# Kernel optimization log

Measured on AMD Instinct MI355X. Metric: run time of the kernel, lower is better.

The kernel has to match this reference:

```python
import jax, jax.numpy as jnp
import numpy as np

T, B, I, H, O = 512, 64, 256, 512, 256

def setup_inputs() -> dict:
    key = jax.random.key(0)
    ks = jax.random.split(key, 7)
    s_ih = 1.0 / np.sqrt(H)
    return {
        "x": jax.random.normal(ks[0], (T, B, I), dtype=jnp.float32),
        "W_ih": jax.random.uniform(ks[1], (H, I), jnp.float32, -s_ih, s_ih),
        "W_hh": jax.random.uniform(ks[2], (H, H), jnp.float32, -s_ih, s_ih),
        "b_ih": jax.random.uniform(ks[3], (H,), jnp.float32, -s_ih, s_ih),
        "b_hh": jax.random.uniform(ks[4], (H,), jnp.float32, -s_ih, s_ih),
        "W_out": jax.random.uniform(ks[5], (O, H), jnp.float32, -s_ih, s_ih),
        "b_out": jax.random.uniform(ks[6], (O,), jnp.float32, -s_ih, s_ih),
    }

def reference(x, W_ih, W_hh, b_ih, b_hh, W_out, b_out):
    # Precompute input projection for all timesteps: [T, B, H]
    xp = jnp.einsum('tbi,hi->tbh', x, W_ih) + b_ih + b_hh

    def step(h, xp_t):
        h_new = jnp.tanh(xp_t + h @ W_hh.T)
        return h_new, h_new

    h0 = jnp.zeros((x.shape[1], W_hh.shape[0]), dtype=x.dtype)
    h_last, rnn_out = jax.lax.scan(step, h0, xp)  # rnn_out: [T, B, H]
    y = jnp.einsum('tbh,oh->tbo', rnn_out, W_out) + b_out
    return y, h_last[None]  # h: [1, B, H] matching torch nn.RNN
```

## Files before the change

kernel.cpp:

```cpp
#include <hip/hip_runtime.h>

#define T_DIM 512
#define B_DIM 64
#define I_DIM 256
#define H_DIM 512
#define O_DIM 256

typedef __attribute__((ext_vector_type(8))) short short8;
typedef __attribute__((ext_vector_type(4))) float f32x4;

__device__ __forceinline__ unsigned short f2bf(float f){
  unsigned int u = __builtin_bit_cast(unsigned int, f);
  u += 0x7fffu + ((u >> 16) & 1u);
  return (unsigned short)(u >> 16);
}
__device__ __forceinline__ float bf2f(unsigned short b){
  unsigned int u = ((unsigned int)b) << 16;
  return __builtin_bit_cast(float, u);
}

#if defined(__has_builtin)
#if __has_builtin(__builtin_amdgcn_sdot4)
#define HAVE_SDOT4 1
#endif
#if __has_builtin(__builtin_amdgcn_update_dpp)
#define HAVE_DPP 1
#endif
#endif

__device__ __forceinline__ int sdot4(int a, int b, int c){
#ifdef HAVE_SDOT4
  return __builtin_amdgcn_sdot4(a, b, c, false);
#else
  #pragma unroll
  for (int i = 0; i < 4; ++i){
    c += (int)(signed char)(a >> (8*i) & 0xff) * (int)(signed char)(b >> (8*i) & 0xff);
  }
  return c;
#endif
}

__device__ __forceinline__ int grp8_sum(int v){
#ifdef HAVE_DPP
  v += __builtin_amdgcn_update_dpp(0, v, 0xB1, 0xf, 0xf, true);
  v += __builtin_amdgcn_update_dpp(0, v, 0x4E, 0xf, 0xf, true);
  v += __builtin_amdgcn_update_dpp(0, v, 0x141, 0xf, 0xf, true);
  return v;
#else
  v += __shfl_xor(v, 1);
  v += __shfl_xor(v, 2);
  v += __shfl_xor(v, 4);
  return v;
#endif
}

__global__ void quant_whh(const float* __restrict__ W, int* __restrict__ Wq){
  int p = blockIdx.x * blockDim.x + threadIdx.x;
  const float s  = 0.04419417382415922f;
  const float qs = 127.0f / s;
  int out = 0;
  #pragma unroll
  for (int i = 0; i < 4; ++i){
    float w = W[(size_t)p*4 + i];
    int q = __float2int_rn(w * qs);
    q = q < -127 ? -127 : (q > 127 ? 127 : q);
    out |= (q & 0xff) << (8*i);
  }
  Wq[p] = out;
}

__global__
__attribute__((amdgpu_flat_work_group_size(1024, 1024)))
void rnn_recur(
    const int* __restrict__ Wq,
    const unsigned short* __restrict__ xp,
    unsigned short* __restrict__ rnn,
    float* __restrict__ hlast)
{
  __shared__ int hq[2][128];
  const int b   = blockIdx.x;
  const int tid = threadIdx.x;
  const int g   = tid >> 3;
  const int c   = tid & 7;
  const int row = 4*g + (c & 3);

  int w[4][16];
  #pragma unroll
  for (int i = 0; i < 4; ++i){
    const uint4* wp = (const uint4*)(Wq + (size_t)(4*g + i)*128 + c*16);
    #pragma unroll
    for (int k = 0; k < 4; ++k){
      uint4 v = wp[k];
      w[i][4*k+0] = (int)v.x; w[i][4*k+1] = (int)v.y;
      w[i][4*k+2] = (int)v.z; w[i][4*k+3] = (int)v.w;
    }
  }
  if (tid < 128) hq[0][tid] = 0;

  const int wj = 4*(g >> 4) + 32*((g >> 2) & 3) + (g & 3);

  const float kscale = 0.04419417382415922f / (127.0f * 127.0f);
  const int BH = B_DIM * H_DIM;

  float xp_next = bf2f(xp[(size_t)b*H_DIM + row]);
  __syncthreads();

  for (int t = 0; t < T_DIM; ++t){
    float xp_cur = xp_next;
    {
      int tn = (t + 1 < T_DIM) ? (t + 1) : t;
      xp_next = bf2f(xp[(size_t)tn*BH + (size_t)b*H_DIM + row]);
    }
    const uint4* hb = (const uint4*)hq[t & 1];
    uint4 hv0 = hb[c];
    uint4 hv1 = hb[c + 8];
    uint4 hv2 = hb[c + 16];
    uint4 hv3 = hb[c + 24];

    int acc[4];
    #pragma unroll
    for (int i = 0; i < 4; ++i) acc[i] = 0;
    #pragma unroll
    for (int i = 0; i < 4; ++i){
      acc[i] = sdot4(w[i][ 0], (int)hv0.x, acc[i]);
      acc[i] = sdot4(w[i][ 1], (int)hv0.y, acc[i]);
      acc[i] = sdot4(w[i][ 2], (int)hv0.z, acc[i]);
      acc[i] = sdot4(w[i][ 3], (int)hv0.w, acc[i]);
      acc[i] = sdot4(w[i][ 4], (int)hv1.x, acc[i]);
      acc[i] = sdot4(w[i][ 5], (int)hv1.y, acc[i]);
      acc[i] = sdot4(w[i][ 6], (int)hv1.z, acc[i]);
      acc[i] = sdot4(w[i][ 7], (int)hv1.w, acc[i]);
      acc[i] = sdot4(w[i][ 8], (int)hv2.x, acc[i]);
      acc[i] = sdot4(w[i][ 9], (int)hv2.y, acc[i]);
      acc[i] = sdot4(w[i][10], (int)hv2.z, acc[i]);
      acc[i] = sdot4(w[i][11], (int)hv2.w, acc[i]);
      acc[i] = sdot4(w[i][12], (int)hv3.x, acc[i]);
      acc[i] = sdot4(w[i][13], (int)hv3.y, acc[i]);
      acc[i] = sdot4(w[i][14], (int)hv3.z, acc[i]);
      acc[i] = sdot4(w[i][15], (int)hv3.w, acc[i]);
    }
    #pragma unroll
    for (int i = 0; i < 4; ++i) acc[i] = grp8_sum(acc[i]);

    int t0 = (c & 1) ? acc[1] : acc[0];
    int t1 = (c & 1) ? acc[3] : acc[2];
    int am = (c & 2) ? t1 : t0;

    float pre = xp_cur + (float)am * kscale;
    float aa = fabsf(pre);
    float e  = __expf(-2.0f * aa);
    float r  = (1.0f - e) * __builtin_amdgcn_rcpf(1.0f + e);
    float h  = copysignf(r, pre);

    if ((tid & 7) < 4){
      rnn[(size_t)t*BH + (size_t)b*H_DIM + row] = f2bf(h);
      if (t == T_DIM - 1) hlast[(size_t)b*H_DIM + row] = h;
    }

    int q = __float2int_rn(h * 127.0f) & 0xff;
#ifdef HAVE_DPP
    int p1 = __builtin_amdgcn_update_dpp(0, q, 0xB1, 0xf, 0xf, true);
    int y  = q | (p1 << 8);
    int p2 = __builtin_amdgcn_update_dpp(0, y, 0x4E, 0xf, 0xf, true);
    int z  = y | (p2 << 16);
    if ((tid & 7) == 0) hq[(t + 1) & 1][wj] = z;
#else
    if ((tid & 7) < 4) ((char*)hq[(t + 1) & 1])[wj*4 + c] = (char)q;
#endif
    __syncthreads();
  }
}

template<typename TA, typename TB, typename TO>
__global__ __launch_bounds__(256) void gemm_bt(
    const TA* __restrict__ A, const TB* __restrict__ B, TO* __restrict__ C,
    const float* __restrict__ bias1, const float* __restrict__ bias2,
    int M, int N, int K)
{
  __shared__ unsigned short As[64][40];
  __shared__ unsigned short Bs[64][40];
  const int tid  = threadIdx.x;
  const int m0   = blockIdx.x * 64;
  const int n0   = blockIdx.y * 64;
  const int srow = tid >> 2, skc = tid & 3;
  const int lane = tid & 63, wid = tid >> 6;
  const int wm   = wid >> 1, wn = wid & 1;
  const int lr   = lane & 15, lq = lane >> 4;

  f32x4 acc[2][2];
  #pragma unroll
  for (int i = 0; i < 2; ++i)
    #pragma unroll
    for (int j = 0; j < 2; ++j) acc[i][j] = (f32x4){0.f, 0.f, 0.f, 0.f};

  for (int k0 = 0; k0 < K; k0 += 32){
    {
      const TA* src = A + (size_t)(m0 + srow)*K + k0 + skc*8;
      uint4 v;
      if constexpr (__is_same(TA, float)){
        float4 f0 = *(const float4*)src;
        float4 f1 = *(const float4*)(src + 4);
        v.x = (unsigned)f2bf(f0.x) | ((unsigned)f2bf(f0.y) << 16);
        v.y = (unsigned)f2bf(f0.z) | ((unsigned)f2bf(f0.w) << 16);
        v.z = (unsigned)f2bf(f1.x) | ((unsigned)f2bf(f1.y) << 16);
        v.w = (unsigned)f2bf(f1.z) | ((unsigned)f2bf(f1.w) << 16);
      } else {
        v = *(const uint4*)src;
      }
      *(uint4*)&As[srow][skc*8] = v;
    }
    {
      const TB* src = B + (size_t)(n0 + srow)*K + k0 + skc*8;
      uint4 v;
      if constexpr (__is_same(TB, float)){
        float4 f0 = *(const float4*)src;
        float4 f1 = *(const float4*)(src + 4);
        v.x = (unsigned)f2bf(f0.x) | ((unsigned)f2bf(f0.y) << 16);
        v.y = (unsigned)f2bf(f0.z) | ((unsigned)f2bf(f0.w) << 16);
        v.z = (unsigned)f2bf(f1.x) | ((unsigned)f2bf(f1.y) << 16);
        v.w = (unsigned)f2bf(f1.z) | ((unsigned)f2bf(f1.w) << 16);
      } else {
        v = *(const uint4*)src;
      }
      *(uint4*)&Bs[srow][skc*8] = v;
    }
    __syncthreads();
    uint4 av0 = *(const uint4*)&As[wm*32      + lr][lq*8];
    uint4 av1 = *(const uint4*)&As[wm*32 + 16 + lr][lq*8];
    uint4 bv0 = *(const uint4*)&Bs[wn*32      + lr][lq*8];
    uint4 bv1 = *(const uint4*)&Bs[wn*32 + 16 + lr][lq*8];
    short8 a0 = __builtin_bit_cast(short8, av0);
    short8 a1 = __builtin_bit_cast(short8, av1);
    short8 b0 = __builtin_bit_cast(short8, bv0);
    short8 b1 = __builtin_bit_cast(short8, bv1);
    acc[0][0] = __builtin_amdgcn_mfma_f32_16x16x32_bf16(a0, b0, acc[0][0], 0, 0, 0);
    acc[0][1] = __builtin_amdgcn_mfma_f32_16x16x32_bf16(a0, b1, acc[0][1], 0, 0, 0);
    acc[1][0] = __builtin_amdgcn_mfma_f32_16x16x32_bf16(a1, b0, acc[1][0], 0, 0, 0);
    acc[1][1] = __builtin_amdgcn_mfma_f32_16x16x32_bf16(a1, b1, acc[1][1], 0, 0, 0);
    __syncthreads();
  }

  #pragma unroll
  for (int i = 0; i < 2; ++i)
    #pragma unroll
    for (int j = 0; j < 2; ++j)
      #pragma unroll
      for (int r = 0; r < 4; ++r){
        int grow = m0 + wm*32 + i*16 + lq*4 + r;
        int gcol = n0 + wn*32 + j*16 + lr;
        float v = acc[i][j][r] + bias1[gcol];
        if (bias2) v += bias2[gcol];
        if constexpr (__is_same(TO, float)) C[(size_t)grow*N + gcol] = v;
        else                                C[(size_t)grow*N + gcol] = f2bf(v);
      }
}

extern "C" void kernel_launch(void* const* d_in, const int* in_sizes, int n_in,
                              void* d_out, int out_size, void* d_ws, size_t ws_size,
                              hipStream_t stream){
  (void)in_sizes; (void)n_in; (void)out_size; (void)ws_size;
  const float* x    = (const float*)d_in[0];
  const float* Wih  = (const float*)d_in[1];
  const float* Whh  = (const float*)d_in[2];
  const float* bih  = (const float*)d_in[3];
  const float* bhh  = (const float*)d_in[4];
  const float* Wout = (const float*)d_in[5];
  const float* bout = (const float*)d_in[6];
  float* y     = (float*)d_out;
  float* hlast = y + (size_t)T_DIM * B_DIM * O_DIM;

  char* ws = (char*)d_ws;
  unsigned short* xp  = (unsigned short*)ws;
  unsigned short* rnn = (unsigned short*)(ws + (size_t)32*1024*1024);
  int*            Wq  = (int*)           (ws + (size_t)64*1024*1024);

  quant_whh<<<256, 256, 0, stream>>>(Whh, Wq);
  gemm_bt<float, float, unsigned short><<<dim3(512, 8), 256, 0, stream>>>(
      x, Wih, xp, bih, bhh, T_DIM*B_DIM, H_DIM, I_DIM);
  rnn_recur<<<64, 1024, 0, stream>>>(Wq, xp, rnn, hlast);
  gemm_bt<unsigned short, float, float><<<dim3(512, 4), 256, 0, stream>>>(
      rnn, Wout, y, bout, nullptr, T_DIM*B_DIM, O_DIM, H_DIM);
}
```

Before: 601.1 us.

## Halve RNN recurrence block size, pre-pack GEMM inputs to bf16, swap grid order

The recurrence kernel now runs 512 threads per batch row instead of 1024. Each thread holds 32 int8 weight words per row and reduces across only 4 lanes, with a swizzled LDS layout and an LDS padding union that limits co-residency. A new pack kernel converts x, W_ih and W_out to bf16 so the GEMMs load 16-bit operands. The GEMM grid is transposed so that blocks sharing the same A rows run adjacently. The trade-off is an extra conversion pass and more registers per recurrence thread, in exchange for cheaper per-step reductions and synchronisation.

```diff
diff --git a/kernel.cpp b/kernel.cpp
--- a/kernel.cpp
+++ b/kernel.cpp
@@ -40,18 +40,23 @@
 #endif
 }
 
-__device__ __forceinline__ int grp8_sum(int v){
-#ifdef HAVE_DPP
-  v += __builtin_amdgcn_update_dpp(0, v, 0xB1, 0xf, 0xf, true);
-  v += __builtin_amdgcn_update_dpp(0, v, 0x4E, 0xf, 0xf, true);
-  v += __builtin_amdgcn_update_dpp(0, v, 0x141, 0xf, 0xf, true);
-  return v;
-#else
-  v += __shfl_xor(v, 1);
-  v += __shfl_xor(v, 2);
-  v += __shfl_xor(v, 4);
-  return v;
-#endif
+__global__ void pack_bf16(const float* __restrict__ x,
+                          const float* __restrict__ wih,
+                          const float* __restrict__ wout,
+                          unsigned short* __restrict__ xb,
+                          unsigned short* __restrict__ wihb,
+                          unsigned short* __restrict__ woutb){
+  const int NX = (T_DIM*B_DIM*I_DIM)/4;
+  const int NW = (H_DIM*I_DIM)/4;
+  int i = blockIdx.x * 256 + threadIdx.x;
+  const float4* src; unsigned short* dst; int j;
+  if (i < NX)          { src = (const float4*)x;    dst = xb;    j = i; }
+  else if (i < NX+NW)  { src = (const float4*)wih;  dst = wihb;  j = i - NX; }
+  else                 { src = (const float4*)wout; dst = woutb; j = i - NX - NW; }
+  float4 f = src[j];
+  ushort4 v;
+  v.x = f2bf(f.x); v.y = f2bf(f.y); v.z = f2bf(f.z); v.w = f2bf(f.w);
+  ((ushort4*)dst)[j] = v;
 }
 
 __global__ void quant_whh(const float* __restrict__ W, int* __restrict__ Wq){
@@ -70,78 +75,88 @@
 }
 
 __global__
-__attribute__((amdgpu_flat_work_group_size(1024, 1024)))
+__attribute__((amdgpu_flat_work_group_size(512, 512), amdgpu_waves_per_eu(2, 2)))
 void rnn_recur(
     const int* __restrict__ Wq,
     const unsigned short* __restrict__ xp,
     unsigned short* __restrict__ rnn,
     float* __restrict__ hlast)
 {
-  __shared__ int hq[2][128];
+  __shared__ union {
+    int  hq[2][128];
+    char occupancy_cap[84 * 1024];
+  } sm;
   const int b   = blockIdx.x;
   const int tid = threadIdx.x;
   const int g   = tid >> 3;
   const int c   = tid & 7;
-  const int row = 4*g + (c & 3);
-
-  int w[4][16];
+  const int cc  = c & 3;
+  const int rr  = c >> 2;
+
+  int w[4][32];
   #pragma unroll
   for (int i = 0; i < 4; ++i){
-    const uint4* wp = (const uint4*)(Wq + (size_t)(4*g + i)*128 + c*16);
-    #pragma unroll
-    for (int k = 0; k < 4; ++k){
+    const uint4* wp = (const uint4*)(Wq + (size_t)(8*g + 4*rr + i)*128 + 32*cc);
+    #pragma unroll
+    for (int k = 0; k < 8; ++k){
       uint4 v = wp[k];
       w[i][4*k+0] = (int)v.x; w[i][4*k+1] = (int)v.y;
       w[i][4*k+2] = (int)v.z; w[i][4*k+3] = (int)v.w;
     }
   }
-  if (tid < 128) hq[0][tid] = 0;
-
-  const int wj = 4*(g >> 4) + 32*((g >> 2) & 3) + (g & 3);
+  if (tid < 256) ((int*)sm.hq)[tid] = 0;
+
+  const int D    = tid >> 2;
+  const int wloc = D ^ (((D >> 5) & 3) << 2);
+
+  int ko[8];
+  #pragma unroll
+  for (int k = 0; k < 8; ++k) ko[k] = 8*cc + (k ^ cc);
 
   const float kscale = 0.04419417382415922f / (127.0f * 127.0f);
   const int BH = B_DIM * H_DIM;
 
-  float xp_next = bf2f(xp[(size_t)b*H_DIM + row]);
+  float xp_next = bf2f(xp[(size_t)b*H_DIM + tid]);
+  float h = 0.0f;
   __syncthreads();
 
   for (int t = 0; t < T_DIM; ++t){
     float xp_cur = xp_next;
     {
       int tn = (t + 1 < T_DIM) ? (t + 1) : t;
-      xp_next = bf2f(xp[(size_t)tn*BH + (size_t)b*H_DIM + row]);
-    }
-    const uint4* hb = (const uint4*)hq[t & 1];
-    uint4 hv0 = hb[c];
-    uint4 hv1 = hb[c + 8];
-    uint4 hv2 = hb[c + 16];
-    uint4 hv3 = hb[c + 24];
+      xp_next = bf2f(xp[(size_t)tn*BH + (size_t)b*H_DIM + tid]);
+    }
+    const uint4* hb = (const uint4*)sm.hq[t & 1];
+    uint4 hv[8];
+    #pragma unroll
+    for (int k = 0; k < 8; ++k) hv[k] = hb[ko[k]];
 
     int acc[4];
     #pragma unroll
     for (int i = 0; i < 4; ++i) acc[i] = 0;
     #pragma unroll
     for (int i = 0; i < 4; ++i){
-      acc[i] = sdot4(w[i][ 0], (int)hv0.x, acc[i]);
-      acc[i] = sdot4(w[i][ 1], (int)hv0.y, acc[i]);
-      acc[i] = sdot4(w[i][ 2], (int)hv0.z, acc[i]);
-      acc[i] = sdot4(w[i][ 3], (int)hv0.w, acc[i]);
-      acc[i] = sdot4(w[i][ 4], (int)hv1.x, acc[i]);
-      acc[i] = sdot4(w[i][ 5], (int)hv1.y, acc[i]);
-      acc[i] = sdot4(w[i][ 6], (int)hv1.z, acc[i]);
-      acc[i] = sdot4(w[i][ 7], (int)hv1.w, acc[i]);
-      acc[i] = sdot4(w[i][ 8], (int)hv2.x, acc[i]);
-      acc[i] = sdot4(w[i][ 9], (int)hv2.y, acc[i]);
-      acc[i] = sdot4(w[i][10], (int)hv2.z, acc[i]);
-      acc[i] = sdot4(w[i][11], (int)hv2.w, acc[i]);
-      acc[i] = sdot4(w[i][12], (int)hv3.x, acc[i]);
-      acc[i] = sdot4(w[i][13], (int)hv3.y, acc[i]);
-      acc[i] = sdot4(w[i][14], (int)hv3.z, acc[i]);
-      acc[i] = sdot4(w[i][15], (int)hv3.w, acc[i]);
-    }
-    #pragma unroll
-    for (int i = 0; i < 4; ++i) acc[i] = grp8_sum(acc[i]);
-
+      #pragma unroll
+      for (int k = 0; k < 8; ++k){
+        acc[i] = sdot4(w[i][4*k+0], (int)hv[k].x, acc[i]);
+        acc[i] = sdot4(w[i][4*k+1], (int)hv[k].y, acc[i]);
+        acc[i] = sdot4(w[i][4*k+2], (int)hv[k].z, acc[i]);
+        acc[i] = sdot4(w[i][4*k+3], (int)hv[k].w, acc[i]);
+      }
+    }
+#ifdef HAVE_DPP
+    #pragma unroll
+    for (int i = 0; i < 4; ++i){
+      acc[i] += __builtin_amdgcn_update_dpp(0, acc[i], 0xB1, 0xf, 0xf, true);
+      acc[i] += __builtin_amdgcn_update_dpp(0, acc[i], 0x4E, 0xf, 0xf, true);
+    }
+#else
+    #pragma unroll
+    for (int i = 0; i < 4; ++i){
+      acc[i] += __shfl_xor(acc[i], 1);
+      acc[i] += __shfl_xor(acc[i], 2);
+    }
+#endif
     int t0 = (c & 1) ? acc[1] : acc[0];
     int t1 = (c & 1) ? acc[3] : acc[2];
     int am = (c & 2) ? t1 : t0;
@@ -150,12 +165,9 @@
     float aa = fabsf(pre);
     float e  = __expf(-2.0f * aa);
     float r  = (1.0f - e) * __builtin_amdgcn_rcpf(1.0f + e);
-    float h  = copysignf(r, pre);
-
-    if ((tid & 7) < 4){
-      rnn[(size_t)t*BH + (size_t)b*H_DIM + row] = f2bf(h);
-      if (t == T_DIM - 1) hlast[(size_t)b*H_DIM + row] = h;
-    }
+    h = copysignf(r, pre);
+
+    rnn[(size_t)t*BH + (size_t)b*H_DIM + tid] = f2bf(h);
 
     int q = __float2int_rn(h * 127.0f) & 0xff;
 #ifdef HAVE_DPP
@@ -163,12 +175,13 @@
     int y  = q | (p1 << 8);
     int p2 = __builtin_amdgcn_update_dpp(0, y, 0x4E, 0xf, 0xf, true);
     int z  = y | (p2 << 16);
-    if ((tid & 7) == 0) hq[(t + 1) & 1][wj] = z;
+    if ((tid & 3) == 0) sm.hq[(t + 1) & 1][wloc] = z;
 #else
-    if ((tid & 7) < 4) ((char*)hq[(t + 1) & 1])[wj*4 + c] = (char)q;
+    ((char*)sm.hq[(t + 1) & 1])[wloc*4 + (tid & 3)] = (char)q;
 #endif
     __syncthreads();
   }
+  hlast[(size_t)b*H_DIM + tid] = h;
 }
 
 template<typename TA, typename TB, typename TO>
@@ -180,8 +193,8 @@
   __shared__ unsigned short As[64][40];
   __shared__ unsigned short Bs[64][40];
   const int tid  = threadIdx.x;
-  const int m0   = blockIdx.x * 64;
-  const int n0   = blockIdx.y * 64;
+  const int m0   = blockIdx.y * 64;
+  const int n0   = blockIdx.x * 64;
   const int srow = tid >> 2, skc = tid & 3;
   const int lane = tid & 63, wid = tid >> 6;
   const int wm   = wid >> 1, wn = wid & 1;
@@ -270,14 +283,19 @@
   float* hlast = y + (size_t)T_DIM * B_DIM * O_DIM;
 
   char* ws = (char*)d_ws;
-  unsigned short* xp  = (unsigned short*)ws;
-  unsigned short* rnn = (unsigned short*)(ws + (size_t)32*1024*1024);
-  int*            Wq  = (int*)           (ws + (size_t)64*1024*1024);
-
+  const size_t MB = 1024*1024;
+  unsigned short* xp   = (unsigned short*)ws;
+  unsigned short* rnn  = (unsigned short*)(ws + 32*MB);
+  unsigned short* xb   = (unsigned short*)(ws + 32*MB);
+  unsigned short* wihb = (unsigned short*)(ws + 48*MB);
+  int*            Wq   = (int*)           (ws + 64*MB);
+  unsigned short* wob  = (unsigned short*)(ws + 64*MB + 256*1024);
+
+  pack_bf16<<<8448, 256, 0, stream>>>(x, Wih, Wout, xb, wihb, wob);
   quant_whh<<<256, 256, 0, stream>>>(Whh, Wq);
-  gemm_bt<float, float, unsigned short><<<dim3(512, 8), 256, 0, stream>>>(
-      x, Wih, xp, bih, bhh, T_DIM*B_DIM, H_DIM, I_DIM);
-  rnn_recur<<<64, 1024, 0, stream>>>(Wq, xp, rnn, hlast);
-  gemm_bt<unsigned short, float, float><<<dim3(512, 4), 256, 0, stream>>>(
-      rnn, Wout, y, bout, nullptr, T_DIM*B_DIM, O_DIM, H_DIM);
-}
+  gemm_bt<unsigned short, unsigned short, unsigned short><<<dim3(8, 512), 256, 0, stream>>>(
+      xb, wihb, xp, bih, bhh, T_DIM*B_DIM, H_DIM, I_DIM);
+  rnn_recur<<<64, 512, 0, stream>>>(Wq, xp, rnn, hlast);
+  gemm_bt<unsigned short, unsigned short, float><<<dim3(4, 512), 256, 0, stream>>>(
+      rnn, wob, y, bout, nullptr, T_DIM*B_DIM, O_DIM, H_DIM);
+}
```

Result: faster. 542.6 us (-9.7%).
